# Kernel optimization log

Hardware: AMD Instinct MI355X
Metric: run time of the kernel (lower is better)

## Reference

```python
import jax, jax.numpy as jnp
import numpy as np

N = 50000   # nodes
E = 800000  # edges (before self loops)
D = 128     # feature dim (n_feat == all n_units due to fusion-cat constraint)
BN_EPS = 1e-5


def _gcn_norm(edge_index, edge_weight, n):
    # PyG gcn_norm with add_self_loops=True (self-loop weight 1.0)
    loop = jnp.arange(n)
    row = jnp.concatenate([edge_index[0], loop])
    col = jnp.concatenate([edge_index[1], loop])
    w = jnp.concatenate([edge_weight, jnp.ones((n,), edge_weight.dtype)])
    deg = jax.ops.segment_sum(w, col, num_segments=n)  # [N]
    deg_safe = jnp.where(deg > 0, deg, 1.0)
    dis = jnp.where(deg > 0, jax.lax.rsqrt(deg_safe), 0.0)
    norm = dis[row] * w * dis[col]  # [E+N]
    return row, col, norm


def _gcn_conv(x, row, col, norm, W, b):
    # out_i = sum_{j->i} norm_ij * (x_j @ W) + b
    h = x @ W                                   # [N, Dout]
    msg = norm[:, None] * h[row]                # gather + scale, [E+N, Dout]
    out = jax.ops.segment_sum(msg, col, num_segments=x.shape[0])
    return out + b


def setup_inputs() -> dict:
    key = jax.random.key(0)
    ks = jax.random.split(key, 9)
    emb = jax.random.normal(ks[0], (N, D), jnp.float32)
    edge_index = jax.random.randint(ks[1], (2, E), 0, N)
    edge_weight = jax.random.uniform(ks[2], (E,), jnp.float32)
    W0 = jax.random.normal(ks[3], (D, D), jnp.float32) / np.sqrt(D).astype(np.float32)
    b0 = jnp.zeros((D,), jnp.float32)
    W1 = jax.random.normal(ks[4], (D, D), jnp.float32) / np.sqrt(D).astype(np.float32)
    b1 = jnp.zeros((D,), jnp.float32)
    bn_gamma = jax.random.uniform(ks[5], (D,), jnp.float32, 0.5, 1.5)
    bn_beta = jax.random.normal(ks[6], (D,), jnp.float32) * 0.1
    bn_mean = jax.random.normal(ks[7], (D,), jnp.float32) * 0.1
    bn_var = jax.random.uniform(ks[8], (D,), jnp.float32, 0.5, 1.5)
    return dict(emb=emb, edge_index=edge_index, edge_weight=edge_weight,
                W0=W0, b0=b0, W1=W1, b1=b1,
                bn_gamma=bn_gamma, bn_beta=bn_beta, bn_mean=bn_mean, bn_var=bn_var)


def reference(emb, edge_index, edge_weight, W0, b0, W1, b1,
              bn_gamma, bn_beta, bn_mean, bn_var):
    n = emb.shape[0]
    row, col, norm = _gcn_norm(edge_index, edge_weight, n)
    # loop runs once (batchnorm_stack has len 1 -> zip truncates):
    h1 = _gcn_conv(emb, row, col, norm, W0, b0)
    h1 = (h1 - bn_mean) * jax.lax.rsqrt(bn_var + BN_EPS) * bn_gamma + bn_beta
    h1 = jax.nn.elu(h1)  # dropout is identity in eval mode
    # final layer applied outside loop, no BN/ELU:
    h2 = _gcn_conv(h1, row, col, norm, W1, b1)
    # fusion: mean over [emb, h1, h2] along the stacked scale axis
    return (emb + h1 + h2) / 3.0
```

## Files before the change

kernel.cpp:

```cpp
#include <hip/hip_runtime.h>
#include <hip/hip_fp16.h>
#include <math.h>

#define BN_EPS 1e-5f
#define CAP 48
#define ABLK 8192

typedef __attribute__((ext_vector_type(8))) short bf16x8;
typedef __attribute__((ext_vector_type(4))) float f32x4;

__device__ __forceinline__ unsigned short f2b(float f) {
    unsigned u = __float_as_uint(f);
    return (unsigned short)((u + 0x7fffu + ((u >> 16) & 1u)) >> 16);
}
__device__ __forceinline__ unsigned pack2(float lo, float hi) {
    return (unsigned)f2b(lo) | ((unsigned)f2b(hi) << 16);
}
__device__ __forceinline__ float slot_w(unsigned s) {
    return __half2float(__ushort_as_half((unsigned short)(s & 0xffffu)));
}
__device__ __forceinline__ float4 b2f4(ushort4 u) {
    return make_float4(__uint_as_float((unsigned)u.x << 16),
                       __uint_as_float((unsigned)u.y << 16),
                       __uint_as_float((unsigned)u.z << 16),
                       __uint_as_float((unsigned)u.w << 16));
}

__global__ __launch_bounds__(1024) void k_bin(
        const int* __restrict__ erow, const int* __restrict__ ecol,
        const float* __restrict__ ew,
        uint2* __restrict__ binned, unsigned short* __restrict__ Hs,
        int E, int NA, int nbins,
        const float* __restrict__ W0, const float* __restrict__ W1,
        const float* __restrict__ emb,
        unsigned short* __restrict__ wp0, unsigned short* __restrict__ wp1,
        unsigned short* __restrict__ embB, int n) {
    int bb = blockIdx.x;
    int t = threadIdx.x;
    if (bb < NA) {
        __shared__ unsigned sHist[256];
        __shared__ unsigned sStart[257];
        __shared__ unsigned sCur[256];
        if (t < 256) sHist[t] = 0;
        __syncthreads();
        int base = bb * ABLK;
        int m = E - base; if (m > ABLK) m = ABLK;
        int er[8]; int ec[8]; float ewt[8];
        int i0 = t * 8;
        if (i0 + 8 <= m) {
            int4 ra = *(const int4*)(erow + base + i0);
            int4 rb = *(const int4*)(erow + base + i0 + 4);
            int4 ca = *(const int4*)(ecol + base + i0);
            int4 cb = *(const int4*)(ecol + base + i0 + 4);
            float4 wa = *(const float4*)(ew + base + i0);
            float4 wb = *(const float4*)(ew + base + i0 + 4);
            er[0] = ra.x; er[1] = ra.y; er[2] = ra.z; er[3] = ra.w;
            er[4] = rb.x; er[5] = rb.y; er[6] = rb.z; er[7] = rb.w;
            ec[0] = ca.x; ec[1] = ca.y; ec[2] = ca.z; ec[3] = ca.w;
            ec[4] = cb.x; ec[5] = cb.y; ec[6] = cb.z; ec[7] = cb.w;
            ewt[0] = wa.x; ewt[1] = wa.y; ewt[2] = wa.z; ewt[3] = wa.w;
            ewt[4] = wb.x; ewt[5] = wb.y; ewt[6] = wb.z; ewt[7] = wb.w;
        } else {
            #pragma unroll
            for (int k = 0; k < 8; ++k) {
                int i = i0 + k;
                if (i < m) { er[k] = erow[base + i]; ec[k] = ecol[base + i]; ewt[k] = ew[base + i]; }
                else { er[k] = 0; ec[k] = -1; ewt[k] = 0.f; }
            }
        }
        #pragma unroll
        for (int k = 0; k < 8; ++k)
            if (ec[k] >= 0) atomicAdd(&sHist[ec[k] >> 8], 1u);
        __syncthreads();
        if (t < 64) {
            unsigned carry = 0;
            #pragma unroll
            for (int c = 0; c < 4; ++c) {
                unsigned v = sHist[c * 64 + t];
                unsigned inc = v;
                #pragma unroll
                for (int d = 1; d < 64; d <<= 1) {
                    unsigned y = __shfl_up(inc, d);
                    if (t >= d) inc += y;
                }
                unsigned ex = carry + inc - v;
                sStart[c * 64 + t] = ex;
                sCur[c * 64 + t] = ex;
                carry += __shfl(inc, 63);
            }
            if (t == 0) sStart[256] = carry;
        }
        __syncthreads();
        if (t <= nbins) Hs[(size_t)bb * 256 + t] = (unsigned short)sStart[t];
        #pragma unroll
        for (int k = 0; k < 8; ++k) {
            if (ec[k] >= 0) {
                int bn = ec[k] >> 8;
                unsigned pos = atomicAdd(&sCur[bn], 1u);
                binned[(size_t)base + pos] =
                    make_uint2(((unsigned)er[k] << 8) | ((unsigned)ec[k] & 255u),
                               __float_as_uint(ewt[k]));
            }
        }
    } else {
        int b2 = bb - NA;
        if (b2 < 4) {
            int tid = b2 * 1024 + t;
            const float* W = (tid < 2048) ? W0 : W1;
            unsigned short* wp = (tid < 2048) ? wp0 : wp1;
            int f = tid & 2047;
            int q = f >> 9;
            int tt = (f >> 6) & 7;
            int l = f & 63;
            int col = tt * 16 + (l & 15);
            int k0 = q * 32 + (l >> 4) * 8;
            unsigned short o[8];
            #pragma unroll
            for (int j = 0; j < 8; ++j) o[j] = f2b(W[(k0 + j) * 128 + col]);
            *(uint4*)(wp + (size_t)f * 8) = *(uint4*)o;
        } else {
            int idx = (b2 - 4) * 1024 + t;
            if (idx < n * 16) {
                const float4* src = (const float4*)emb + (size_t)idx * 2;
                float4 v0 = src[0], v1 = src[1];
                uint4 o;
                o.x = pack2(v0.x, v0.y); o.y = pack2(v0.z, v0.w);
                o.z = pack2(v1.x, v1.y); o.w = pack2(v1.z, v1.w);
                ((uint4*)embB)[idx] = o;
            }
        }
    }
}

__global__ __launch_bounds__(1024) void k_build(
        const uint2* __restrict__ binned, const unsigned short* __restrict__ Hs,
        int NA, unsigned* __restrict__ eEdge, int* __restrict__ cnt,
        float* __restrict__ dis, int n) {
    __shared__ unsigned cntL[256];
    __shared__ float wsumL[256];
    int t = threadIdx.x;
    if (t < 256) { cntL[t] = 0; wsumL[t] = 0.f; }
    __syncthreads();
    int b = blockIdx.x;
    int node0 = b << 8;
    int wv = t >> 6, lane = t & 63;
    for (int s = wv; s < NA; s += 16) {
        int start = Hs[(size_t)s * 256 + b];
        int end   = Hs[(size_t)s * 256 + b + 1];
        size_t sb = (size_t)s * ABLK;
        for (int o = start + lane; o < end; o += 64) {
            uint2 rec = binned[sb + o];
            unsigned d = rec.x & 255u;
            unsigned r = rec.x >> 8;
            float w = __uint_as_float(rec.y);
            unsigned p = atomicAdd(&cntL[d], 1u);
            if (p < CAP)
                eEdge[(size_t)(node0 + (int)d) * CAP + p] =
                    (r << 16) | (unsigned)__half_as_ushort(__float2half(w));
            atomicAdd(&wsumL[d], w);
        }
    }
    __syncthreads();
    if (t < 256) {
        int node = node0 + t;
        if (node < n) {
            unsigned c = cntL[t]; if (c > CAP) c = CAP;
            cnt[node] = (int)c;
            dis[node] = rsqrtf(wsumL[t] + 1.0f);
        }
    }
}

__device__ __forceinline__ void agg_node(const unsigned* __restrict__ ep,
                                         const unsigned short* __restrict__ h,
                                         const float* __restrict__ dis,
                                         float disc, int c, int lane,
                                         float acc[8]) {
    int g = lane >> 4;
    int fo = (lane & 15) * 8;
    for (int j = 0; j < c; j += 16) {
        unsigned s[4];
        int r[4];
        float d[4], nm[4];
        uint4 u[4];
        #pragma unroll
        for (int k = 0; k < 4; ++k) s[k] = ep[j + 4 * k + g];
        #pragma unroll
        for (int k = 0; k < 4; ++k) r[k] = (j + 4 * k + g < c) ? (int)(s[k] >> 16) : 0;
        #pragma unroll
        for (int k = 0; k < 4; ++k) d[k] = dis[r[k]];
        #pragma unroll
        for (int k = 0; k < 4; ++k) u[k] = *(const uint4*)(h + ((size_t)r[k] << 7) + fo);
        #pragma unroll
        for (int k = 0; k < 4; ++k)
            nm[k] = (j + 4 * k + g < c) ? d[k] * slot_w(s[k]) * disc : 0.f;
        #pragma unroll
        for (int k = 0; k < 4; ++k) {
            acc[0] += nm[k] * __uint_as_float(u[k].x << 16);
            acc[1] += nm[k] * __uint_as_float(u[k].x & 0xffff0000u);
            acc[2] += nm[k] * __uint_as_float(u[k].y << 16);
            acc[3] += nm[k] * __uint_as_float(u[k].y & 0xffff0000u);
            acc[4] += nm[k] * __uint_as_float(u[k].z << 16);
            acc[5] += nm[k] * __uint_as_float(u[k].z & 0xffff0000u);
            acc[6] += nm[k] * __uint_as_float(u[k].w << 16);
            acc[7] += nm[k] * __uint_as_float(u[k].w & 0xffff0000u);
        }
    }
    #pragma unroll
    for (int f = 0; f < 8; ++f) {
        acc[f] += __shfl_xor(acc[f], 16);
        acc[f] += __shfl_xor(acc[f], 32);
    }
}

__global__ __launch_bounds__(1024) void k_conv1(
        const int* __restrict__ cnt, const unsigned* __restrict__ eEdge,
        const unsigned short* __restrict__ embB, const float* __restrict__ dis,
        const unsigned short* __restrict__ wp,
        const float* __restrict__ b0, const float* __restrict__ gamma,
        const float* __restrict__ beta, const float* __restrict__ mean,
        const float* __restrict__ var,
        unsigned short* __restrict__ h1b, int n) {
    __shared__ unsigned short sWp[16384];
    __shared__ unsigned short sA[16 * 136];
    int t = threadIdx.x;
    { uint4* d = (uint4*)sWp; const uint4* s = (const uint4*)wp;
      d[t] = s[t]; d[t + 1024] = s[t + 1024]; }
    int w = t >> 6;
    int lane = t & 63;
    int wid = blockIdx.x * 16 + w;
    bool valid = wid < n;
    int c = valid ? __builtin_amdgcn_readfirstlane(cnt[wid]) : 0;
    float disc = valid ? dis[wid] : 0.f;
    float acc[8] = {};
    agg_node(eEdge + (size_t)wid * CAP, embB, dis, disc, c, lane, acc);
    if (lane < 16) {
        int fo = lane * 8;
        float s2 = disc * disc;
        uint4 hu = make_uint4(0, 0, 0, 0);
        if (valid) hu = *(const uint4*)(embB + ((size_t)wid << 7) + fo);
        acc[0] += s2 * __uint_as_float(hu.x << 16);
        acc[1] += s2 * __uint_as_float(hu.x & 0xffff0000u);
        acc[2] += s2 * __uint_as_float(hu.y << 16);
        acc[3] += s2 * __uint_as_float(hu.y & 0xffff0000u);
        acc[4] += s2 * __uint_as_float(hu.z << 16);
        acc[5] += s2 * __uint_as_float(hu.z & 0xffff0000u);
        acc[6] += s2 * __uint_as_float(hu.w << 16);
        acc[7] += s2 * __uint_as_float(hu.w & 0xffff0000u);
        uint4 o;
        o.x = pack2(acc[0], acc[1]); o.y = pack2(acc[2], acc[3]);
        o.z = pack2(acc[4], acc[5]); o.w = pack2(acc[6], acc[7]);
        *(uint4*)(sA + w * 136 + fo) = o;
    }
    __syncthreads();
    int m = lane & 15, quad = lane >> 4;
    f32x4 c2 = {0.f, 0.f, 0.f, 0.f};
    if (w < 8) {
        #pragma unroll
        for (int q = 0; q < 4; ++q) {
            bf16x8 a = *(const bf16x8*)(sA + m * 136 + q * 32 + quad * 8);
            bf16x8 b = *(const bf16x8*)(sWp + (size_t)((q * 8 + w) * 64 + lane) * 8);
            c2 = __builtin_amdgcn_mfma_f32_16x16x32_bf16(a, b, c2, 0, 0, 0);
        }
    }
    __syncthreads();
    if (w < 8) {
        int col = w * 16 + m;
        float bias = b0[col];
        float mn = mean[col], bt = beta[col];
        float iv = rsqrtf(var[col] + BN_EPS) * gamma[col];
        #pragma unroll
        for (int r = 0; r < 4; ++r) {
            float x = c2[r] + bias;
            x = (x - mn) * iv + bt;
            x = x > 0.f ? x : expm1f(x);
            sA[(quad * 4 + r) * 136 + col] = f2b(x);
        }
    }
    __syncthreads();
    if (t < 256) {
        int r = t >> 4, c8 = (t & 15) * 8;
        int node = blockIdx.x * 16 + r;
        if (node < n)
            *(uint4*)(h1b + ((size_t)node << 7) + c8) = *(const uint4*)(sA + r * 136 + c8);
    }
}

__global__ __launch_bounds__(1024) void k_conv2(
        const int* __restrict__ cnt, const unsigned* __restrict__ eEdge,
        const unsigned short* __restrict__ h1b, const float* __restrict__ dis,
        const unsigned short* __restrict__ wp,
        const float* __restrict__ b1, const float* __restrict__ emb,
        float* __restrict__ out, int n) {
    __shared__ unsigned short sWp[16384];
    __shared__ unsigned short sA[16 * 136];
    __shared__ float sC[16 * 132];
    int t = threadIdx.x;
    { uint4* d = (uint4*)sWp; const uint4* s = (const uint4*)wp;
      d[t] = s[t]; d[t + 1024] = s[t + 1024]; }
    int w = t >> 6;
    int lane = t & 63;
    int wid = blockIdx.x * 16 + w;
    bool valid = wid < n;
    int c = valid ? __builtin_amdgcn_readfirstlane(cnt[wid]) : 0;
    float disc = valid ? dis[wid] : 0.f;
    float acc[8] = {};
    agg_node(eEdge + (size_t)wid * CAP, h1b, dis, disc, c, lane, acc);
    if (lane < 16) {
        int fo = lane * 8;
        float s2 = disc * disc;
        uint4 hu = make_uint4(0, 0, 0, 0);
        if (valid) hu = *(const uint4*)(h1b + ((size_t)wid << 7) + fo);
        acc[0] += s2 * __uint_as_float(hu.x << 16);
        acc[1] += s2 * __uint_as_float(hu.x & 0xffff0000u);
        acc[2] += s2 * __uint_as_float(hu.y << 16);
        acc[3] += s2 * __uint_as_float(hu.y & 0xffff0000u);
        acc[4] += s2 * __uint_as_float(hu.z << 16);
        acc[5] += s2 * __uint_as_float(hu.z & 0xffff0000u);
        acc[6] += s2 * __uint_as_float(hu.w << 16);
        acc[7] += s2 * __uint_as_float(hu.w & 0xffff0000u);
        uint4 o;
        o.x = pack2(acc[0], acc[1]); o.y = pack2(acc[2], acc[3]);
        o.z = pack2(acc[4], acc[5]); o.w = pack2(acc[6], acc[7]);
        *(uint4*)(sA + w * 136 + fo) = o;
    }
    __syncthreads();
    int m = lane & 15, quad = lane >> 4;
    f32x4 c2 = {0.f, 0.f, 0.f, 0.f};
    if (w < 8) {
        #pragma unroll
        for (int q = 0; q < 4; ++q) {
            bf16x8 a = *(const bf16x8*)(sA + m * 136 + q * 32 + quad * 8);
            bf16x8 b = *(const bf16x8*)(sWp + (size_t)((q * 8 + w) * 64 + lane) * 8);
            c2 = __builtin_amdgcn_mfma_f32_16x16x32_bf16(a, b, c2, 0, 0, 0);
        }
        int col = w * 16 + m;
        float bias = b1[col];
        #pragma unroll
        for (int r = 0; r < 4; ++r)
            sC[(quad * 4 + r) * 132 + col] = c2[r] + bias;
    }
    __syncthreads();
    if (t < 512) {
        int r = t >> 5, c4 = (t & 31) * 4;
        int node = blockIdx.x * 16 + r;
        if (node < n) {
            float4 cc = *(const float4*)(sC + r * 132 + c4);
            float4 ev = *(const float4*)(emb + ((size_t)node << 7) + c4);
            float4 hv = b2f4(*(const ushort4*)(h1b + ((size_t)node << 7) + c4));
            const float third = 1.0f / 3.0f;
            float4 o;
            o.x = (ev.x + hv.x + cc.x) * third;
            o.y = (ev.y + hv.y + cc.y) * third;
            o.z = (ev.z + hv.z + cc.z) * third;
            o.w = (ev.w + hv.w + cc.w) * third;
            *(float4*)(out + ((size_t)node << 7) + c4) = o;
        }
    }
}

extern "C" void kernel_launch(void* const* d_in, const int* in_sizes, int n_in,
                              void* d_out, int out_size, void* d_ws, size_t ws_size,
                              hipStream_t stream) {
    const float* emb   = (const float*)d_in[0];
    const int*   eidx  = (const int*)d_in[1];
    const float* ew    = (const float*)d_in[2];
    const float* W0    = (const float*)d_in[3];
    const float* b0    = (const float*)d_in[4];
    const float* W1    = (const float*)d_in[5];
    const float* b1    = (const float*)d_in[6];
    const float* gamma = (const float*)d_in[7];
    const float* beta  = (const float*)d_in[8];
    const float* mean  = (const float*)d_in[9];
    const float* var   = (const float*)d_in[10];

    const int n = in_sizes[0] / 128;
    const int E = in_sizes[2];
    const int* rowp = eidx;
    const int* colp = eidx + E;

    char* ws = (char*)d_ws;
    unsigned short* embB = (unsigned short*)ws;
    unsigned short* h1b  = (unsigned short*)(ws + (size_t)n * 256);
    uint2* binned = (uint2*)h1b;
    char* p = ws + (size_t)n * 512;
    float* dis  = (float*)p;
    int*   cnt  = (int*)  (p + (size_t)n * 4);
    unsigned short* wp0 = (unsigned short*)(p + (size_t)n * 8);
    unsigned short* wp1 = (unsigned short*)(p + (size_t)n * 8 + 32768);
    unsigned short* Hs  = (unsigned short*)(p + (size_t)n * 8 + 65536);
    unsigned* eEdge = (unsigned*)(p + (size_t)n * 8 + 131072);
    float* outf = (float*)d_out;

    const int NA    = (E + ABLK - 1) / ABLK;
    const int PB    = 4 + (n * 16 + 1023) / 1024;
    const int nbins = (n + 255) >> 8;
    const int cb    = (n + 15) / 16;

    k_bin<<<NA + PB, 1024, 0, stream>>>(rowp, colp, ew, binned, Hs, E, NA, nbins,
                                        W0, W1, emb, wp0, wp1, embB, n);
    k_build<<<nbins, 1024, 0, stream>>>(binned, Hs, NA, eEdge, cnt, dis, n);
    k_conv1<<<cb, 1024, 0, stream>>>(cnt, eEdge, embB, dis, wp0,
                                     b0, gamma, beta, mean, var, h1b, n);
    k_conv2<<<cb, 1024, 0, stream>>>(cnt, eEdge, h1b, dis, wp1,
                                     b1, emb, outf, n);
}
```

Before: 199.7 us.

## Bin edges by 16-node groups and build per-block edge lists inside conv kernels

Measured after the change: 211.7 us. +6.0%, slower.

```diff
diff --git a/kernel.cpp b/kernel.cpp
--- a/kernel.cpp
+++ b/kernel.cpp
@@ -15,9 +15,6 @@
 }
 __device__ __forceinline__ unsigned pack2(float lo, float hi) {
     return (unsigned)f2b(lo) | ((unsigned)f2b(hi) << 16);
-}
-__device__ __forceinline__ float slot_w(unsigned s) {
-    return __half2float(__ushort_as_half((unsigned short)(s & 0xffffu)));
 }
 __device__ __forceinline__ float4 b2f4(ushort4 u) {
     return make_float4(__uint_as_float((unsigned)u.x << 16),
@@ -29,8 +26,8 @@
 __global__ __launch_bounds__(1024) void k_bin(
         const int* __restrict__ erow, const int* __restrict__ ecol,
         const float* __restrict__ ew,
-        uint2* __restrict__ binned, unsigned short* __restrict__ Hs,
-        int E, int NA, int nbins,
+        uint2* __restrict__ binned, unsigned* __restrict__ HsSE,
+        int E, int NA, int hsw,
         const float* __restrict__ W0, const float* __restrict__ W1,
         const float* __restrict__ emb,
         unsigned short* __restrict__ wp0, unsigned short* __restrict__ wp1,
@@ -38,10 +35,11 @@
     int bb = blockIdx.x;
     int t = threadIdx.x;
     if (bb < NA) {
-        __shared__ unsigned sHist[256];
-        __shared__ unsigned sStart[257];
-        __shared__ unsigned sCur[256];
-        if (t < 256) sHist[t] = 0;
+        __shared__ unsigned sHist[3152];
+        __shared__ unsigned sStart[3153];
+        __shared__ unsigned sWs[16];
+        __shared__ uint2 sRec[ABLK];
+        for (int b = t; b < 3152; b += 1024) sHist[b] = 0;
         __syncthreads();
         int base = bb * ABLK;
         int m = E - base; if (m > ABLK) m = ABLK;
@@ -70,38 +68,47 @@
         }
         #pragma unroll
         for (int k = 0; k < 8; ++k)
-            if (ec[k] >= 0) atomicAdd(&sHist[ec[k] >> 8], 1u);
-        __syncthreads();
-        if (t < 64) {
-            unsigned carry = 0;
-            #pragma unroll
-            for (int c = 0; c < 4; ++c) {
-                unsigned v = sHist[c * 64 + t];
-                unsigned inc = v;
-                #pragma unroll
-                for (int d = 1; d < 64; d <<= 1) {
-                    unsigned y = __shfl_up(inc, d);
-                    if (t >= d) inc += y;
-                }
-                unsigned ex = carry + inc - v;
-                sStart[c * 64 + t] = ex;
-                sCur[c * 64 + t] = ex;
-                carry += __shfl(inc, 63);
-            }
-            if (t == 0) sStart[256] = carry;
-        }
-        __syncthreads();
-        if (t <= nbins) Hs[(size_t)bb * 256 + t] = (unsigned short)sStart[t];
+            if (ec[k] >= 0) atomicAdd(&sHist[ec[k] >> 4], 1u);
+        __syncthreads();
+        int lane = t & 63, wid = t >> 6;
+        unsigned v0 = 0, v1 = 0, v2 = 0, v3 = 0, sum = 0;
+        int b0 = t * 4;
+        if (b0 < 3152) {
+            v0 = sHist[b0]; v1 = sHist[b0 + 1]; v2 = sHist[b0 + 2]; v3 = sHist[b0 + 3];
+            sum = v0 + v1 + v2 + v3;
+        }
+        unsigned inc = sum;
+        #pragma unroll
+        for (int d = 1; d < 64; d <<= 1) {
+            unsigned y = __shfl_up(inc, d);
+            if (lane >= d) inc += y;
+        }
+        if (lane == 63) sWs[wid] = inc;
+        __syncthreads();
+        unsigned woff = 0;
+        for (int ww = 0; ww < wid; ++ww) woff += sWs[ww];
+        unsigned ex = woff + inc - sum;
+        if (b0 < 3152) {
+            sStart[b0] = ex;
+            sStart[b0 + 1] = ex + v0;
+            sStart[b0 + 2] = ex + v0 + v1;
+            sStart[b0 + 3] = ex + v0 + v1 + v2;
+        }
+        __syncthreads();
+        for (int b = t; b < hsw; b += 1024)
+            HsSE[(size_t)b * NA + bb] = (sStart[b] & 0xffffu) | (sStart[b + 1] << 16);
+        for (int b = t; b < 3152; b += 1024) sHist[b] = sStart[b];
+        __syncthreads();
         #pragma unroll
         for (int k = 0; k < 8; ++k) {
             if (ec[k] >= 0) {
-                int bn = ec[k] >> 8;
-                unsigned pos = atomicAdd(&sCur[bn], 1u);
-                binned[(size_t)base + pos] =
-                    make_uint2(((unsigned)er[k] << 8) | ((unsigned)ec[k] & 255u),
-                               __float_as_uint(ewt[k]));
-            }
-        }
+                unsigned pos = atomicAdd(&sHist[ec[k] >> 4], 1u);
+                sRec[pos] = make_uint2(((unsigned)er[k] << 8) | ((unsigned)ec[k] & 255u),
+                                       __float_as_uint(ewt[k]));
+            }
+        }
+        __syncthreads();
+        for (int i = t; i < m; i += 1024) binned[(size_t)base + i] = sRec[i];
     } else {
         int b2 = bb - NA;
         if (b2 < 4) {
@@ -132,108 +139,105 @@
     }
 }
 
-__global__ __launch_bounds__(1024) void k_build(
-        const uint2* __restrict__ binned, const unsigned short* __restrict__ Hs,
-        int NA, unsigned* __restrict__ eEdge, int* __restrict__ cnt,
-        float* __restrict__ dis, int n) {
-    __shared__ unsigned cntL[256];
+__global__ __launch_bounds__(1024) void k_deg(
+        const uint2* __restrict__ binned, const unsigned* __restrict__ HsSE,
+        int NA, float* __restrict__ dis, int n) {
     __shared__ float wsumL[256];
     int t = threadIdx.x;
-    if (t < 256) { cntL[t] = 0; wsumL[t] = 0.f; }
-    __syncthreads();
-    int b = blockIdx.x;
-    int node0 = b << 8;
-    int wv = t >> 6, lane = t & 63;
-    for (int s = wv; s < NA; s += 16) {
-        int start = Hs[(size_t)s * 256 + b];
-        int end   = Hs[(size_t)s * 256 + b + 1];
+    if (t < 256) wsumL[t] = 0.f;
+    __syncthreads();
+    int g = blockIdx.x;
+    int b0 = g * 16;
+    int wid = t >> 6, lane = t & 63;
+    for (int s = wid; s < NA; s += 16) {
+        unsigned va = HsSE[(size_t)b0 * NA + s];
+        unsigned vb = HsSE[(size_t)(b0 + 15) * NA + s];
+        int start = (int)(va & 0xffffu);
+        int end = (int)(vb >> 16);
         size_t sb = (size_t)s * ABLK;
         for (int o = start + lane; o < end; o += 64) {
             uint2 rec = binned[sb + o];
-            unsigned d = rec.x & 255u;
-            unsigned r = rec.x >> 8;
-            float w = __uint_as_float(rec.y);
-            unsigned p = atomicAdd(&cntL[d], 1u);
-            if (p < CAP)
-                eEdge[(size_t)(node0 + (int)d) * CAP + p] =
-                    (r << 16) | (unsigned)__half_as_ushort(__float2half(w));
-            atomicAdd(&wsumL[d], w);
+            atomicAdd(&wsumL[rec.x & 255u], __uint_as_float(rec.y));
         }
     }
     __syncthreads();
     if (t < 256) {
-        int node = node0 + t;
-        if (node < n) {
-            unsigned c = cntL[t]; if (c > CAP) c = CAP;
-            cnt[node] = (int)c;
-            dis[node] = rsqrtf(wsumL[t] + 1.0f);
-        }
-    }
-}
-
-__device__ __forceinline__ void agg_node(const unsigned* __restrict__ ep,
-                                         const unsigned short* __restrict__ h,
-                                         const float* __restrict__ dis,
-                                         float disc, int c, int lane,
-                                         float acc[8]) {
-    int g = lane >> 4;
-    int fo = (lane & 15) * 8;
-    for (int j = 0; j < c; j += 16) {
-        unsigned s[4];
-        int r[4];
-        float d[4], nm[4];
-        uint4 u[4];
-        #pragma unroll
-        for (int k = 0; k < 4; ++k) s[k] = ep[j + 4 * k + g];
-        #pragma unroll
-        for (int k = 0; k < 4; ++k) r[k] = (j + 4 * k + g < c) ? (int)(s[k] >> 16) : 0;
-        #pragma unroll
-        for (int k = 0; k < 4; ++k) d[k] = dis[r[k]];
-        #pragma unroll
-        for (int k = 0; k < 4; ++k) u[k] = *(const uint4*)(h + ((size_t)r[k] << 7) + fo);
-        #pragma unroll
-        for (int k = 0; k < 4; ++k)
-            nm[k] = (j + 4 * k + g < c) ? d[k] * slot_w(s[k]) * disc : 0.f;
-        #pragma unroll
-        for (int k = 0; k < 4; ++k) {
-            acc[0] += nm[k] * __uint_as_float(u[k].x << 16);
-            acc[1] += nm[k] * __uint_as_float(u[k].x & 0xffff0000u);
-            acc[2] += nm[k] * __uint_as_float(u[k].y << 16);
-            acc[3] += nm[k] * __uint_as_float(u[k].y & 0xffff0000u);
-            acc[4] += nm[k] * __uint_as_float(u[k].z << 16);
-            acc[5] += nm[k] * __uint_as_float(u[k].z & 0xffff0000u);
-            acc[6] += nm[k] * __uint_as_float(u[k].w << 16);
-            acc[7] += nm[k] * __uint_as_float(u[k].w & 0xffff0000u);
-        }
-    }
-    #pragma unroll
-    for (int f = 0; f < 8; ++f) {
-        acc[f] += __shfl_xor(acc[f], 16);
-        acc[f] += __shfl_xor(acc[f], 32);
+        int node = g * 256 + t;
+        if (node < n) dis[node] = rsqrtf(wsumL[t] + 1.0f);
     }
 }
 
 __global__ __launch_bounds__(1024) void k_conv1(
-        const int* __restrict__ cnt, const unsigned* __restrict__ eEdge,
-        const unsigned short* __restrict__ embB, const float* __restrict__ dis,
-        const unsigned short* __restrict__ wp,
-        const float* __restrict__ b0, const float* __restrict__ gamma,
+        const uint2* __restrict__ binned, const unsigned* __restrict__ HsSE,
+        int NA, const unsigned short* __restrict__ embB,
+        const float* __restrict__ dis, const unsigned short* __restrict__ wp,
+        const float* __restrict__ b0v, const float* __restrict__ gamma,
         const float* __restrict__ beta, const float* __restrict__ mean,
         const float* __restrict__ var,
         unsigned short* __restrict__ h1b, int n) {
     __shared__ unsigned short sWp[16384];
     __shared__ unsigned short sA[16 * 136];
+    __shared__ unsigned short sR[16 * CAP];
+    __shared__ float sW[16 * CAP];
+    __shared__ unsigned sCnt[16];
     int t = threadIdx.x;
     { uint4* d = (uint4*)sWp; const uint4* s = (const uint4*)wp;
       d[t] = s[t]; d[t + 1024] = s[t + 1024]; }
+    if (t < 16) sCnt[t] = 0;
+    __syncthreads();
+    int bin = blockIdx.x;
+    for (int s = t >> 3; s < NA; s += 128) {
+        unsigned v = HsSE[(size_t)bin * NA + s];
+        int start = (int)(v & 0xffffu), end = (int)(v >> 16);
+        size_t sb = (size_t)s * ABLK;
+        for (int i = start + (t & 7); i < end; i += 8) {
+            uint2 rec = binned[sb + i];
+            unsigned d16 = rec.x & 15u;
+            unsigned r = rec.x >> 8;
+            float wd = __uint_as_float(rec.y) * dis[r];
+            unsigned pos = atomicAdd(&sCnt[d16], 1u);
+            if (pos < CAP) { sR[d16 * CAP + pos] = (unsigned short)r; sW[d16 * CAP + pos] = wd; }
+        }
+    }
+    __syncthreads();
     int w = t >> 6;
     int lane = t & 63;
-    int wid = blockIdx.x * 16 + w;
+    int wid = bin * 16 + w;
     bool valid = wid < n;
-    int c = valid ? __builtin_amdgcn_readfirstlane(cnt[wid]) : 0;
+    int c = (int)sCnt[w]; if (c > CAP) c = CAP;
     float disc = valid ? dis[wid] : 0.f;
     float acc[8] = {};
-    agg_node(eEdge + (size_t)wid * CAP, embB, dis, disc, c, lane, acc);
+    {
+        int g2 = lane >> 4;
+        int fo = (lane & 15) * 8;
+        for (int j = 0; j < c; j += 16) {
+            int r[4]; float nm[4]; uint4 u[4];
+            #pragma unroll
+            for (int k = 0; k < 4; ++k) {
+                int idx = j + 4 * k + g2;
+                r[k] = (idx < c) ? (int)sR[w * CAP + idx] : 0;
+                nm[k] = (idx < c) ? sW[w * CAP + idx] * disc : 0.f;
+            }
+            #pragma unroll
+            for (int k = 0; k < 4; ++k) u[k] = *(const uint4*)(embB + ((size_t)r[k] << 7) + fo);
+            #pragma unroll
+            for (int k = 0; k < 4; ++k) {
+                acc[0] += nm[k] * __uint_as_float(u[k].x << 16);
+                acc[1] += nm[k] * __uint_as_float(u[k].x & 0xffff0000u);
+                acc[2] += nm[k] * __uint_as_float(u[k].y << 16);
+                acc[3] += nm[k] * __uint_as_float(u[k].y & 0xffff0000u);
+                acc[4] += nm[k] * __uint_as_float(u[k].z << 16);
+                acc[5] += nm[k] * __uint_as_float(u[k].z & 0xffff0000u);
+                acc[6] += nm[k] * __uint_as_float(u[k].w << 16);
+                acc[7] += nm[k] * __uint_as_float(u[k].w & 0xffff0000u);
+            }
+        }
+        #pragma unroll
+        for (int f = 0; f < 8; ++f) {
+            acc[f] += __shfl_xor(acc[f], 16);
+            acc[f] += __shfl_xor(acc[f], 32);
+        }
+    }
     if (lane < 16) {
         int fo = lane * 8;
         float s2 = disc * disc;
@@ -253,20 +257,20 @@
         *(uint4*)(sA + w * 136 + fo) = o;
     }
     __syncthreads();
-    int m = lane & 15, quad = lane >> 4;
+    int mm = lane & 15, quad = lane >> 4;
     f32x4 c2 = {0.f, 0.f, 0.f, 0.f};
     if (w < 8) {
         #pragma unroll
         for (int q = 0; q < 4; ++q) {
-            bf16x8 a = *(const bf16x8*)(sA + m * 136 + q * 32 + quad * 8);
+            bf16x8 a = *(const bf16x8*)(sA + mm * 136 + q * 32 + quad * 8);
             bf16x8 b = *(const bf16x8*)(sWp + (size_t)((q * 8 + w) * 64 + lane) * 8);
             c2 = __builtin_amdgcn_mfma_f32_16x16x32_bf16(a, b, c2, 0, 0, 0);
         }
     }
     __syncthreads();
     if (w < 8) {
-        int col = w * 16 + m;
-        float bias = b0[col];
+        int col = w * 16 + mm;
+        float bias = b0v[col];
         float mn = mean[col], bt = beta[col];
         float iv = rsqrtf(var[col] + BN_EPS) * gamma[col];
         #pragma unroll
@@ -280,32 +284,82 @@
     __syncthreads();
     if (t < 256) {
         int r = t >> 4, c8 = (t & 15) * 8;
-        int node = blockIdx.x * 16 + r;
+        int node = bin * 16 + r;
         if (node < n)
             *(uint4*)(h1b + ((size_t)node << 7) + c8) = *(const uint4*)(sA + r * 136 + c8);
     }
 }
 
 __global__ __launch_bounds__(1024) void k_conv2(
-        const int* __restrict__ cnt, const unsigned* __restrict__ eEdge,
-        const unsigned short* __restrict__ h1b, const float* __restrict__ dis,
-        const unsigned short* __restrict__ wp,
-        const float* __restrict__ b1, const float* __restrict__ emb,
+        const uint2* __restrict__ binned, const unsigned* __restrict__ HsSE,
+        int NA, const unsigned short* __restrict__ h1b,
+        const float* __restrict__ dis, const unsigned short* __restrict__ wp,
+        const float* __restrict__ b1v, const float* __restrict__ emb,
         float* __restrict__ out, int n) {
     __shared__ unsigned short sWp[16384];
     __shared__ unsigned short sA[16 * 136];
     __shared__ float sC[16 * 132];
+    __shared__ unsigned short sR[16 * CAP];
+    __shared__ float sW[16 * CAP];
+    __shared__ unsigned sCnt[16];
     int t = threadIdx.x;
     { uint4* d = (uint4*)sWp; const uint4* s = (const uint4*)wp;
       d[t] = s[t]; d[t + 1024] = s[t + 1024]; }
+    if (t < 16) sCnt[t] = 0;
+    __syncthreads();
+    int bin = blockIdx.x;
+    for (int s = t >> 3; s < NA; s += 128) {
+        unsigned v = HsSE[(size_t)bin * NA + s];
+        int start = (int)(v & 0xffffu), end = (int)(v >> 16);
+        size_t sb = (size_t)s * ABLK;
+        for (int i = start + (t & 7); i < end; i += 8) {
+            uint2 rec = binned[sb + i];
+            unsigned d16 = rec.x & 15u;
+            unsigned r = rec.x >> 8;
+            float wd = __uint_as_float(rec.y) * dis[r];
+            unsigned pos = atomicAdd(&sCnt[d16], 1u);
+            if (pos < CAP) { sR[d16 * CAP + pos] = (unsigned short)r; sW[d16 * CAP + pos] = wd; }
+        }
+    }
+    __syncthreads();
     int w = t >> 6;
     int lane = t & 63;
-    int wid = blockIdx.x * 16 + w;
+    int wid = bin * 16 + w;
     bool valid = wid < n;
-    int c = valid ? __builtin_amdgcn_readfirstlane(cnt[wid]) : 0;
+    int c = (int)sCnt[w]; if (c > CAP) c = CAP;
     float disc = valid ? dis[wid] : 0.f;
     float acc[8] = {};
-    agg_node(eEdge + (size_t)wid * CAP, h1b, dis, disc, c, lane, acc);
+    {
+        int g2 = lane >> 4;
+        int fo = (lane & 15) * 8;
+        for (int j = 0; j < c; j += 16) {
+            int r[4]; float nm[4]; uint4 u[4];
+            #pragma unroll
+            for (int k = 0; k < 4; ++k) {
+                int idx = j + 4 * k + g2;
+                r[k] = (idx < c) ? (int)sR[w * CAP + idx] : 0;
+                nm[k] = (idx < c) ? sW[w * CAP + idx] * disc : 0.f;
+            }
+            #pragma unroll
+            for (int k = 0; k < 4; ++k) u[k] = *(const uint4*)(h1b + ((size_t)r[k] << 7) + fo);
+            #pragma unroll
+            for (int k = 0; k < 4; ++k) {
+                acc[0] += nm[k] * __uint_as_float(u[k].x << 16);
+                acc[1] += nm[k] * __uint_as_float(u[k].x & 0xffff0000u);
+                acc[2] += nm[k] * __uint_as_float(u[k].y << 16);
+                acc[3] += nm[k] * __uint_as_float(u[k].y & 0xffff0000u);
+                acc[4] += nm[k] * __uint_as_float(u[k].z << 16);
+                acc[5] += nm[k] * __uint_as_float(u[k].z & 0xffff0000u);
+                acc[6] += nm[k] * __uint_as_float(u[k].w << 16);
+                acc[7] += nm[k] * __uint_as_float(u[k].w & 0xffff0000u);
+            }
+        }
+        #pragma unroll
+        for (int f = 0; f < 8; ++f) {
+            acc[f] += __shfl_xor(acc[f], 16);
+            acc[f] += __shfl_xor(acc[f], 32);
+        }
+    }
     if (lane < 16) {
         int fo = lane * 8;
         float s2 = disc * disc;
@@ -325,17 +379,17 @@
         *(uint4*)(sA + w * 136 + fo) = o;
     }
     __syncthreads();
-    int m = lane & 15, quad = lane >> 4;
+    int mm = lane & 15, quad = lane >> 4;
     f32x4 c2 = {0.f, 0.f, 0.f, 0.f};
     if (w < 8) {
         #pragma unroll
         for (int q = 0; q < 4; ++q) {
-            bf16x8 a = *(const bf16x8*)(sA + m * 136 + q * 32 + quad * 8);
+            bf16x8 a = *(const bf16x8*)(sA + mm * 136 + q * 32 + quad * 8);
             bf16x8 b = *(const bf16x8*)(sWp + (size_t)((q * 8 + w) * 64 + lane) * 8);
             c2 = __builtin_amdgcn_mfma_f32_16x16x32_bf16(a, b, c2, 0, 0, 0);
         }
-        int col = w * 16 + m;
-        float bias = b1[col];
+        int col = w * 16 + mm;
+        float bias = b1v[col];
         #pragma unroll
         for (int r = 0; r < 4; ++r)
             sC[(quad * 4 + r) * 132 + col] = c2[r] + bias;
@@ -343,7 +397,7 @@
     __syncthreads();
     if (t < 512) {
         int r = t >> 5, c4 = (t & 31) * 4;
-        int node = blockIdx.x * 16 + r;
+        int node = bin * 16 + r;
         if (node < n) {
             float4 cc = *(const float4*)(sC + r * 132 + c4);
             float4 ev = *(const float4*)(emb + ((size_t)node << 7) + c4);
@@ -379,29 +433,30 @@
     const int* rowp = eidx;
     const int* colp = eidx + E;
 
+    const int NA    = (E + ABLK - 1) / ABLK;
+    const int nbins = (n + 15) / 16;
+    const int hsw   = ((nbins + 16) / 16) * 16;
+    const int PB    = 4 + (n * 16 + 1023) / 1024;
+    const int gb    = (n + 255) / 256;
+
     char* ws = (char*)d_ws;
     unsigned short* embB = (unsigned short*)ws;
     unsigned short* h1b  = (unsigned short*)(ws + (size_t)n * 256);
-    uint2* binned = (uint2*)h1b;
     char* p = ws + (size_t)n * 512;
-    float* dis  = (float*)p;
-    int*   cnt  = (int*)  (p + (size_t)n * 4);
-    unsigned short* wp0 = (unsigned short*)(p + (size_t)n * 8);
-    unsigned short* wp1 = (unsigned short*)(p + (size_t)n * 8 + 32768);
-    unsigned short* Hs  = (unsigned short*)(p + (size_t)n * 8 + 65536);
-    unsigned* eEdge = (unsigned*)(p + (size_t)n * 8 + 131072);
+    float* dis = (float*)p;
+    size_t o = ((size_t)n * 4 + 255) & ~(size_t)255;
+    unsigned short* wp0 = (unsigned short*)(p + o);
+    unsigned short* wp1 = (unsigned short*)(p + o + 32768);
+    unsigned* HsSE = (unsigned*)(p + o + 65536);
+    size_t o2 = o + 65536 + (((size_t)hsw * NA * 4 + 255) & ~(size_t)255);
+    uint2* binned = (uint2*)(p + o2);
     float* outf = (float*)d_out;
 
-    const int NA    = (E + ABLK - 1) / ABLK;
-    const int PB    = 4 + (n * 16 + 1023) / 1024;
-    const int nbins = (n + 255) >> 8;
-    const int cb    = (n + 15) / 16;
-
-    k_bin<<<NA + PB, 1024, 0, stream>>>(rowp, colp, ew, binned, Hs, E, NA, nbins,
+    k_bin<<<NA + PB, 1024, 0, stream>>>(rowp, colp, ew, binned, HsSE, E, NA, hsw,
                                         W0, W1, emb, wp0, wp1, embB, n);
-    k_build<<<nbins, 1024, 0, stream>>>(binned, Hs, NA, eEdge, cnt, dis, n);
-    k_conv1<<<cb, 1024, 0, stream>>>(cnt, eEdge, embB, dis, wp0,
-                                     b0, gamma, beta, mean, var, h1b, n);
-    k_conv2<<<cb, 1024, 0, stream>>>(cnt, eEdge, h1b, dis, wp1,
-                                     b1, emb, outf, n);
-}
+    k_deg<<<gb, 1024, 0, stream>>>(binned, HsSE, NA, dis, n);
+    k_conv1<<<nbins, 1024, 0, stream>>>(binned, HsSE, NA, embB, dis, wp0,
+                                        b0, gamma, beta, mean, var, h1b, n);
+    k_conv2<<<nbins, 1024, 0, stream>>>(binned, HsSE, NA, h1b, dis, wp1,
+                                        b1, emb, outf, n);
+}
```
